# Optimization experiments

Measured on AMD Instinct MI355X. Metric: run time of the kernel, lower is better.

The kernel has to match this reference:

```python
import jax, jax.numpy as jnp
import numpy as np

N_CHANNELS = 256
N_NEIGHBOURS = 262144
DIM = 3


def setup_inputs() -> dict:
    key = jax.random.key(0)
    k1, k2, k3 = jax.random.split(key, 3)
    h = jax.random.normal(k1, (N_CHANNELS, N_NEIGHBOURS), dtype=jnp.float32)
    rel_poss = jax.random.normal(k2, (DIM, N_NEIGHBOURS), dtype=jnp.float32)
    W = jax.random.normal(k3, (N_CHANNELS, N_CHANNELS), dtype=jnp.float32)
    return {"h": h, "rel_poss": rel_poss, "W": W}


def reference(h, rel_poss, W):
    # dists: [N], unit directions u: [dim, N]
    dists = jnp.linalg.norm(rel_poss, axis=0)
    u = rel_poss / dists
    # radial basis e_rbf(x, n, c=2) = (2/2)**0.5 * sin(n*x)/x = sin(n*x)/x, n = 1..K
    n = jnp.arange(1, N_CHANNELS + 1, dtype=h.dtype)
    radial_emb = jnp.sin(n[:, None] * dists[None, :]) / dists[None, :]  # [K, N]
    # channel-mixed features
    hp = W @ h  # [K, N]
    # per-neighbour: radial * feature scalar times rank-2 outer product u u^T, summed over neighbours
    m = radial_emb * hp  # [K, N]
    A = jnp.einsum('ki,di,ei->kde', m, u, u)  # [K, dim, dim]
    return A
```

## Files before the change

kernel.cpp:

```cpp
#include <hip/hip_runtime.h>
#include <hip/hip_bf16.h>

#define NCH      256
#define NNB      262144
#define BN       64
#define NTILES   (NNB / BN)
#define NB       512
#define ITPB     (NTILES / NB)
#define NENT     (NCH * 6)
#define NTHREADS 512

typedef __bf16        bf16x8 __attribute__((ext_vector_type(8)));
typedef float         f32x4  __attribute__((ext_vector_type(4)));
typedef unsigned int  u32x4  __attribute__((ext_vector_type(4)));
typedef unsigned int  u32x2  __attribute__((ext_vector_type(2)));
typedef short         v4s    __attribute__((ext_vector_type(4)));

union FragU  { u32x4 u; bf16x8 b; };
union Frag2U { u32x2 u; v4s    s; };

__device__ __forceinline__ unsigned pk2(float lo, float hi) {
    union { __hip_bfloat162 h2; unsigned u; } cv;
    cv.h2 = __float22bfloat162_rn(make_float2(lo, hi));
    return cv.u;
}

__device__ __forceinline__ const float* uni_ptr(const float* p) {
    unsigned long long u = (unsigned long long)p;
    unsigned lo = __builtin_amdgcn_readfirstlane((unsigned)u);
    unsigned hi = __builtin_amdgcn_readfirstlane((unsigned)(u >> 32));
    return (const float*)(((unsigned long long)hi << 32) | lo);
}

#define LBAR() do {                                                  \
    asm volatile("s_waitcnt lgkmcnt(0)" ::: "memory");               \
    __builtin_amdgcn_sched_barrier(0);                               \
    __builtin_amdgcn_s_barrier();                                    \
    __builtin_amdgcn_sched_barrier(0);                               \
} while (0)

#define CBODY(CB, P)                                                               \
{                                                                                  \
    const int colb = (CB) * 16;                                                    \
    Frag2U gf;                                                                     \
    gf.u = *(const u32x2*)((const char*)gT[P] +                                    \
           (((unsigned)(il * 128 + (colb + q * 4) * 2)) ^                          \
            (((unsigned)(il & 7)) << 3)));                                         \
    f32x4 hp0 = {0.f, 0.f, 0.f, 0.f}, hp1 = {0.f, 0.f, 0.f, 0.f};                  \
    const unsigned rb = (unsigned)((colb + il) * 512);                             \
    const unsigned sw = ((unsigned)(il & 7)) << 4;                                 \
    _Pragma("unroll")                                                              \
    for (int jb = 0; jb < 8; ++jb) {                                               \
        FragU f0;                                                                  \
        f0.u = *(const u32x4*)((const char*)htile[P] +                             \
               ((rb + (unsigned)(jb * 64 + q * 16)) ^ sw));                        \
        hp0 = __builtin_amdgcn_mfma_f32_16x16x32_bf16(f0.b, wf[0][jb].b, hp0, 0, 0, 0); \
        hp1 = __builtin_amdgcn_mfma_f32_16x16x32_bf16(f0.b, wf[1][jb].b, hp1, 0, 0, 0); \
    }                                                                              \
    f32x4 d4 = *(const f32x4*)&dtab[P][0][colb + q * 4];                           \
    f32x4 i4 = *(const f32x4*)&dtab[P][1][colb + q * 4];                           \
    Frag2U a0, a1;                                                                 \
    {                                                                              \
        float m0 = __sinf(fk0 * d4[0]) * i4[0] * hp0[0];                           \
        float m1 = __sinf(fk0 * d4[1]) * i4[1] * hp0[1];                           \
        float m2 = __sinf(fk0 * d4[2]) * i4[2] * hp0[2];                           \
        float m3 = __sinf(fk0 * d4[3]) * i4[3] * hp0[3];                           \
        a0.u[0] = pk2(m0, m1); a0.u[1] = pk2(m2, m3);                              \
        float n0 = __sinf(fk1 * d4[0]) * i4[0] * hp1[0];                           \
        float n1 = __sinf(fk1 * d4[1]) * i4[1] * hp1[1];                           \
        float n2 = __sinf(fk1 * d4[2]) * i4[2] * hp1[2];                           \
        float n3 = __sinf(fk1 * d4[3]) * i4[3] * hp1[3];                           \
        a1.u[0] = pk2(n0, n1); a1.u[1] = pk2(n2, n3);                              \
    }                                                                              \
    acc0 = __builtin_amdgcn_mfma_f32_16x16x16bf16_1k(a0.s, gf.s, acc0, 0, 0, 0);   \
    acc1 = __builtin_amdgcn_mfma_f32_16x16x16bf16_1k(a1.s, gf.s, acc1, 0, 0, 0);   \
}

#define ITER(P, CUR, NXT, TILE_EXPR)                                               \
{                                                                                  \
    const int tile = (TILE_EXPR);                                                  \
    const int tn1  = tile + NB;                                                    \
    const int tn2  = tile + 2 * NB;                                                \
    const unsigned ii1 = (unsigned)(((tn1 < NTILES) ? tn1 : tile) * BN) + (unsigned)c; \
    {                                                    \
        const int lt = (tn2 < NTILES) ? tn2 : tile;                                \
        const unsigned ii = (unsigned)(lt * BN) + (unsigned)c;                     \
        NXT[0] = rp[ii];                                                           \
        NXT[1] = rp[(size_t)NNB + ii];                                             \
        NXT[2] = rp[2 * (size_t)NNB + ii];                                         \
    }                                                                              \
    float hA[16];                                                                  \
    if (tn1 < NTILES) {         \
        _Pragma("unroll")                                                          \
        for (int j = 0; j < 16; ++j) hA[j] = hwb[(size_t)j * NNB + ii1];           \
    }                                                                              \
    __builtin_amdgcn_sched_barrier(0);                                             \
    CBODY(0, P)                                                                    \
    CBODY(1, P)                                                                    \
    __builtin_amdgcn_sched_barrier(0);                                             \
    float hB[16];                                                                  \
    if (tn1 < NTILES) {                                                            \
                       \
        u32x4 w0, w1;                                                              \
        w0[0] = pk2(hA[0], hA[1]);   w0[1] = pk2(hA[2], hA[3]);                    \
        w0[2] = pk2(hA[4], hA[5]);   w0[3] = pk2(hA[6], hA[7]);                    \
        w1[0] = pk2(hA[8], hA[9]);   w1[1] = pk2(hA[10], hA[11]);                  \
        w1[2] = pk2(hA[12], hA[13]); w1[3] = pk2(hA[14], hA[15]);                  \
        const unsigned swc = ((unsigned)(c & 7)) << 4;                             \
        *(u32x4*)((char*)htile[(P) ^ 1] +                                          \
                  (((unsigned)(c * 512 + wave * 64)) ^ swc)) = w0;                 \
        *(u32x4*)((char*)htile[(P) ^ 1] +                                          \
                  (((unsigned)(c * 512 + wave * 64 + 16)) ^ swc)) = w1;            \
        _Pragma("unroll")                                                          \
        for (int j = 0; j < 16; ++j) hB[j] = hwb[(size_t)(16 + j) * NNB + ii1];    \
    }                                                                              \
    __builtin_amdgcn_sched_barrier(0);                                             \
    CBODY(2, P)                                                                    \
    CBODY(3, P)                                                                    \
    __builtin_amdgcn_sched_barrier(0);                                             \
    if (tn1 < NTILES) {      \
        u32x4 w2, w3;                                                              \
        w2[0] = pk2(hB[0], hB[1]);   w2[1] = pk2(hB[2], hB[3]);                    \
        w2[2] = pk2(hB[4], hB[5]);   w2[3] = pk2(hB[6], hB[7]);                    \
        w3[0] = pk2(hB[8], hB[9]);   w3[1] = pk2(hB[10], hB[11]);                  \
        w3[2] = pk2(hB[12], hB[13]); w3[3] = pk2(hB[14], hB[15]);                  \
        const unsigned swc = ((unsigned)(c & 7)) << 4;                             \
        *(u32x4*)((char*)htile[(P) ^ 1] +                                          \
                  (((unsigned)(c * 512 + wave * 64 + 32)) ^ swc)) = w2;            \
        *(u32x4*)((char*)htile[(P) ^ 1] +                                          \
                  (((unsigned)(c * 512 + wave * 64 + 48)) ^ swc)) = w3;            \
        float dd = sqrtf(CUR[0] * CUR[0] + CUR[1] * CUR[1] + CUR[2] * CUR[2]);     \
        float iv = 1.0f / dd;                                                      \
        if (t < 64) {                                                              \
            dtab[(P) ^ 1][0][c] = dd;                                              \
            dtab[(P) ^ 1][1][c] = iv;                                              \
            float i2 = iv * iv;                                                    \
            float gg[6] = { CUR[0] * CUR[0] * i2, CUR[0] * CUR[1] * i2,            \
                            CUR[0] * CUR[2] * i2, CUR[1] * CUR[1] * i2,            \
                            CUR[1] * CUR[2] * i2, CUR[2] * CUR[2] * i2 };          \
            _Pragma("unroll")                                                      \
            for (int de = 0; de < 6; ++de) {                                       \
                unsigned off = ((unsigned)(de * 128 + c * 2)) ^                    \
                               (((unsigned)de) << 3);                              \
                *(unsigned short*)((char*)gT[(P) ^ 1] + off) =                     \
                    (unsigned short)(pk2(gg[de], 0.f) & 0xffffu);                  \
            }                                                                      \
        }                                                                          \
    }                                                                              \
    LBAR();                                                                        \
}

__global__ __launch_bounds__(NTHREADS, 2) void create_As_k1(
        const float* __restrict__ h, const float* __restrict__ rp,
        const float* __restrict__ W, float* __restrict__ ws)
{
    __shared__ unsigned short htile[2][BN * NCH];
    __shared__ unsigned short gT[2][16 * BN];
    __shared__ __align__(16) float dtab[2][2][BN];

    const int t    = threadIdx.x;
    const int wave = t >> 6;
    const int il   = t & 15;
    const int q    = (t >> 4) & 3;
    const int c    = t & 63;
    const int k0   = wave * 32;
    const float fk0 = (float)(k0 + il + 1);
    const float fk1 = fk0 + 16.0f;

    #pragma unroll
    for (int z = 0; z < 4; ++z) ((unsigned*)gT)[t + z * NTHREADS] = 0u;

    FragU wf[2][8];
    #pragma unroll
    for (int kt = 0; kt < 2; ++kt) {
        const float* wr = W + (size_t)(k0 + kt * 16 + il) * NCH + q * 8;
        #pragma unroll
        for (int jb = 0; jb < 8; ++jb) {
            f32x4 a = *(const f32x4*)(wr + jb * 32);
            f32x4 b = *(const f32x4*)(wr + jb * 32 + 4);
            wf[kt][jb].u[0] = pk2(a[0], a[1]);
            wf[kt][jb].u[1] = pk2(a[2], a[3]);
            wf[kt][jb].u[2] = pk2(b[0], b[1]);
            wf[kt][jb].u[3] = pk2(b[2], b[3]);
        }
    }

    f32x4 acc0 = {0.f, 0.f, 0.f, 0.f};
    f32x4 acc1 = {0.f, 0.f, 0.f, 0.f};

    const float* hwb = uni_ptr(h + (size_t)(wave * 32) * NNB);

    float pA[3], pB[3];
    const int tile0 = blockIdx.x;

    __syncthreads();

    {
        const unsigned ii = (unsigned)(tile0 * BN) + (unsigned)c;
        pB[0] = rp[ii]; pB[1] = rp[(size_t)NNB + ii]; pB[2] = rp[2 * (size_t)NNB + ii];
        float hv[32];
        #pragma unroll
        for (int j = 0; j < 32; ++j) hv[j] = hwb[(size_t)j * NNB + ii];

        const unsigned swc = ((unsigned)(c & 7)) << 4;
        #pragma unroll
        for (int g2 = 0; g2 < 4; ++g2) {
            u32x4 w0;
            w0[0] = pk2(hv[g2 * 8 + 0], hv[g2 * 8 + 1]);
            w0[1] = pk2(hv[g2 * 8 + 2], hv[g2 * 8 + 3]);
            w0[2] = pk2(hv[g2 * 8 + 4], hv[g2 * 8 + 5]);
            w0[3] = pk2(hv[g2 * 8 + 6], hv[g2 * 8 + 7]);
            *(u32x4*)((char*)htile[0] +
                      (((unsigned)(c * 512 + wave * 64 + g2 * 16)) ^ swc)) = w0;
        }

        float dd = sqrtf(pB[0] * pB[0] + pB[1] * pB[1] + pB[2] * pB[2]);
        float iv = 1.0f / dd;
        if (t < 64) {
            dtab[0][0][c] = dd; dtab[0][1][c] = iv;
            float i2 = iv * iv;
            float gg[6] = { pB[0] * pB[0] * i2, pB[0] * pB[1] * i2, pB[0] * pB[2] * i2,
                            pB[1] * pB[1] * i2, pB[1] * pB[2] * i2, pB[2] * pB[2] * i2 };
            #pragma unroll
            for (int de = 0; de < 6; ++de) {
                unsigned off = ((unsigned)(de * 128 + c * 2)) ^ (((unsigned)de) << 3);
                *(unsigned short*)((char*)gT[0] + off) =
                    (unsigned short)(pk2(gg[de], 0.f) & 0xffffu);
            }
        }
        const unsigned i1 = (unsigned)((tile0 + NB) * BN) + (unsigned)c;
        pA[0] = rp[i1]; pA[1] = rp[(size_t)NNB + i1]; pA[2] = rp[2 * (size_t)NNB + i1];
    }
    LBAR();

    #pragma unroll 1
    for (int it2 = 0; it2 < ITPB; it2 += 2) {
        const int tb = tile0 + it2 * NB;
        ITER(0, pA, pB, tb)
        ITER(1, pB, pA, tb + NB)
    }

    if (il < 6) {
        float* dst = ws + (size_t)blockIdx.x * NENT;
        #pragma unroll
        for (int r = 0; r < 4; ++r) {
            dst[(k0 + q * 4 + r) * 6 + il]      = acc0[r];
            dst[(k0 + 16 + q * 4 + r) * 6 + il] = acc1[r];
        }
    }
}

__global__ void create_As_k2(const float* __restrict__ ws, float* __restrict__ out)
{
    __shared__ float red[8][64];
    const int eb = blockIdx.x;
    const int w  = threadIdx.x >> 6;
    const int l  = threadIdx.x & 63;
    float s = 0.f;
    #pragma unroll 4
    for (int b = w; b < NB; b += 8)
        s += ws[(size_t)b * NENT + (unsigned)(eb * 64 + l)];
    red[w][l] = s;
    __syncthreads();
    if (w == 0) {
        float v = red[0][l] + red[1][l] + red[2][l] + red[3][l]
                + red[4][l] + red[5][l] + red[6][l] + red[7][l];
        const int e  = eb * 64 + l;
        const int k  = e / 6;
        const int m6 = e - k * 6;
        const int d  = (m6 < 3) ? 0 : ((m6 < 5) ? 1 : 2);
        const int e2 = (m6 < 3) ? m6 : ((m6 < 5) ? (m6 - 2) : 2);
        out[k * 9 + d * 3 + e2] = v;
        if (d != e2) out[k * 9 + e2 * 3 + d] = v;
    }
}

extern "C" void kernel_launch(void* const* d_in, const int* in_sizes, int n_in,
                              void* d_out, int out_size, void* d_ws, size_t ws_size,
                              hipStream_t stream)
{
    const float* h  = (const float*)d_in[0];
    const float* rp = (const float*)d_in[1];
    const float* W  = (const float*)d_in[2];
    float* out = (float*)d_out;
    float* ws  = (float*)d_ws;

    hipLaunchKernelGGL(create_As_k1, dim3(NB), dim3(NTHREADS), 0, stream, h, rp, W, ws);
    hipLaunchKernelGGL(create_As_k2, dim3(NENT / 64), dim3(512), 0, stream, ws, out);
}
```

Baseline: 84.01 us.

## Double neighbour tile to 128 with one resident block per CU

Result: slower. 209.9 us (+149.8%).

```diff
diff --git a/kernel.cpp b/kernel.cpp
--- a/kernel.cpp
+++ b/kernel.cpp
@@ -3,10 +3,10 @@
 
 #define NCH      256
 #define NNB      262144
-#define BN       64
-#define NTILES   (NNB / BN)
-#define NB       512
-#define ITPB     (NTILES / NB)
+#define BN       128
+#define NDT      (NNB / BN)
+#define NB       256
+#define DTPB     (NDT / NB)
 #define NENT     (NCH * 6)
 #define NTHREADS 512
 
@@ -44,7 +44,7 @@
     const int colb = (CB) * 16;                                                    \
     Frag2U gf;                                                                     \
     gf.u = *(const u32x2*)((const char*)gT[P] +                                    \
-           (((unsigned)(il * 128 + (colb + q * 4) * 2)) ^                          \
+           (((unsigned)(il * 256 + (colb + q * 4) * 2)) ^                          \
             (((unsigned)(il & 7)) << 3)));                                         \
     f32x4 hp0 = {0.f, 0.f, 0.f, 0.f}, hp1 = {0.f, 0.f, 0.f, 0.f};                  \
     const unsigned rb = (unsigned)((colb + il) * 512);                             \
@@ -76,71 +76,66 @@
     acc1 = __builtin_amdgcn_mfma_f32_16x16x16bf16_1k(a1.s, gf.s, acc1, 0, 0, 0);   \
 }
 
-#define ITER(P, CUR, NXT, TILE_EXPR)                                               \
+#define ITER(P, CUR, NXT, DT_EXPR)                                                 \
 {                                                                                  \
-    const int tile = (TILE_EXPR);                                                  \
-    const int tn1  = tile + NB;                                                    \
-    const int tn2  = tile + 2 * NB;                                                \
-    const unsigned ii1 = (unsigned)(((tn1 < NTILES) ? tn1 : tile) * BN) + (unsigned)c; \
+    const int dt  = (DT_EXPR);                                                     \
+    const int dn1 = dt + NB;                                                       \
+    const int dn2 = dt + 2 * NB;                                                   \
+    const unsigned base1 = (unsigned)(((dn1 < NDT) ? dn1 : dt) * BN);              \
     {                                                    \
-        const int lt = (tn2 < NTILES) ? tn2 : tile;                                \
-        const unsigned ii = (unsigned)(lt * BN) + (unsigned)c;                     \
+        const int lt = (dn2 < NDT) ? dn2 : dt;                                     \
+        const unsigned ii = (unsigned)(lt * BN) + (unsigned)(t & 127);             \
         NXT[0] = rp[ii];                                                           \
         NXT[1] = rp[(size_t)NNB + ii];                                             \
         NXT[2] = rp[2 * (size_t)NNB + ii];                                         \
     }                                                                              \
-    float hA[16];                                                                  \
-    if (tn1 < NTILES) {         \
+    float hv0[32], hv1[32];                                                        \
+    if (dn1 < NDT) {                                                               \
         _Pragma("unroll")                                                          \
-        for (int j = 0; j < 16; ++j) hA[j] = hwb[(size_t)j * NNB + ii1];           \
+        for (int j = 0; j < 32; ++j) {                                             \
+            hv0[j] = hwb[(size_t)j * NNB + base1 + l];                             \
+            hv1[j] = hwb[(size_t)j * NNB + base1 + l + 64];                        \
+        }                                                                          \
     }                                                                              \
     __builtin_amdgcn_sched_barrier(0);                                             \
-    CBODY(0, P)                                                                    \
-    CBODY(1, P)                                                                    \
+    CBODY(0, P) CBODY(1, P) CBODY(2, P) CBODY(3, P)                                \
+    CBODY(4, P) CBODY(5, P) CBODY(6, P) CBODY(7, P)                                \
     __builtin_amdgcn_sched_barrier(0);                                             \
-    float hB[16];                                                                  \
-    if (tn1 < NTILES) {                                                            \
-                       \
-        u32x4 w0, w1;                                                              \
-        w0[0] = pk2(hA[0], hA[1]);   w0[1] = pk2(hA[2], hA[3]);                    \
-        w0[2] = pk2(hA[4], hA[5]);   w0[3] = pk2(hA[6], hA[7]);                    \
-        w1[0] = pk2(hA[8], hA[9]);   w1[1] = pk2(hA[10], hA[11]);                  \
-        w1[2] = pk2(hA[12], hA[13]); w1[3] = pk2(hA[14], hA[15]);                  \
-        const unsigned swc = ((unsigned)(c & 7)) << 4;                             \
-        *(u32x4*)((char*)htile[(P) ^ 1] +                                          \
-                  (((unsigned)(c * 512 + wave * 64)) ^ swc)) = w0;                 \
-        *(u32x4*)((char*)htile[(P) ^ 1] +                                          \
-                  (((unsigned)(c * 512 + wave * 64 + 16)) ^ swc)) = w1;            \
+    if (dn1 < NDT) {                                                               \
+        const unsigned swp = ((unsigned)(l & 7)) << 4;                             \
         _Pragma("unroll")                                                          \
-        for (int j = 0; j < 16; ++j) hB[j] = hwb[(size_t)(16 + j) * NNB + ii1];    \
-    }                                                                              \
-    __builtin_amdgcn_sched_barrier(0);                                             \
-    CBODY(2, P)                                                                    \
-    CBODY(3, P)                                                                    \
-    __builtin_amdgcn_sched_barrier(0);                                             \
-    if (tn1 < NTILES) {      \
-        u32x4 w2, w3;                                                              \
-        w2[0] = pk2(hB[0], hB[1]);   w2[1] = pk2(hB[2], hB[3]);                    \
-        w2[2] = pk2(hB[4], hB[5]);   w2[3] = pk2(hB[6], hB[7]);                    \
-        w3[0] = pk2(hB[8], hB[9]);   w3[1] = pk2(hB[10], hB[11]);                  \
-        w3[2] = pk2(hB[12], hB[13]); w3[3] = pk2(hB[14], hB[15]);                  \
-        const unsigned swc = ((unsigned)(c & 7)) << 4;                             \
-        *(u32x4*)((char*)htile[(P) ^ 1] +                                          \
-                  (((unsigned)(c * 512 + wave * 64 + 32)) ^ swc)) = w2;            \
-        *(u32x4*)((char*)htile[(P) ^ 1] +                                          \
-                  (((unsigned)(c * 512 + wave * 64 + 48)) ^ swc)) = w3;            \
-        float dd = sqrtf(CUR[0] * CUR[0] + CUR[1] * CUR[1] + CUR[2] * CUR[2]);     \
-        float iv = 1.0f / dd;                                                      \
-        if (t < 64) {                                                              \
-            dtab[(P) ^ 1][0][c] = dd;                                              \
-            dtab[(P) ^ 1][1][c] = iv;                                              \
+        for (int g2 = 0; g2 < 4; ++g2) {                                           \
+            u32x4 w0;                                                              \
+            w0[0] = pk2(hv0[g2 * 8 + 0], hv0[g2 * 8 + 1]);                         \
+            w0[1] = pk2(hv0[g2 * 8 + 2], hv0[g2 * 8 + 3]);                         \
+            w0[2] = pk2(hv0[g2 * 8 + 4], hv0[g2 * 8 + 5]);                         \
+            w0[3] = pk2(hv0[g2 * 8 + 6], hv0[g2 * 8 + 7]);                         \
+            *(u32x4*)((char*)htile[(P) ^ 1] +                                      \
+                      (((unsigned)(l * 512 + wave * 64 + g2 * 16)) ^ swp)) = w0;   \
+        }                                                                          \
+        _Pragma("unroll")                                                          \
+        for (int g2 = 0; g2 < 4; ++g2) {                                           \
+            u32x4 w1;                                                              \
+            w1[0] = pk2(hv1[g2 * 8 + 0], hv1[g2 * 8 + 1]);                         \
+            w1[1] = pk2(hv1[g2 * 8 + 2], hv1[g2 * 8 + 3]);                         \
+            w1[2] = pk2(hv1[g2 * 8 + 4], hv1[g2 * 8 + 5]);                         \
+            w1[3] = pk2(hv1[g2 * 8 + 6], hv1[g2 * 8 + 7]);                         \
+            *(u32x4*)((char*)htile[(P) ^ 1] +                                      \
+                      (((unsigned)((l + 64) * 512 + wave * 64 + g2 * 16)) ^ swp)) = w1; \
+        }                                                                          \
+        if (t < 128) {                        \
+            const int cc = t;                                                      \
+            float dd = sqrtf(CUR[0] * CUR[0] + CUR[1] * CUR[1] + CUR[2] * CUR[2]); \
+            float iv = 1.0f / dd;                                                  \
+            dtab[(P) ^ 1][0][cc] = dd;                                             \
+            dtab[(P) ^ 1][1][cc] = iv;                                             \
             float i2 = iv * iv;                                                    \
             float gg[6] = { CUR[0] * CUR[0] * i2, CUR[0] * CUR[1] * i2,            \
                             CUR[0] * CUR[2] * i2, CUR[1] * CUR[1] * i2,            \
                             CUR[1] * CUR[2] * i2, CUR[2] * CUR[2] * i2 };          \
             _Pragma("unroll")                                                      \
             for (int de = 0; de < 6; ++de) {                                       \
-                unsigned off = ((unsigned)(de * 128 + c * 2)) ^                    \
+                unsigned off = ((unsigned)(de * 256 + cc * 2)) ^                   \
                                (((unsigned)de) << 3);                              \
                 *(unsigned short*)((char*)gT[(P) ^ 1] + off) =                     \
                     (unsigned short)(pk2(gg[de], 0.f) & 0xffffu);                  \
@@ -150,7 +145,7 @@
     LBAR();                                                                        \
 }
 
-__global__ __launch_bounds__(NTHREADS, 2) void create_As_k1(
+__global__ __launch_bounds__(NTHREADS, 1) void create_As_k1(
         const float* __restrict__ h, const float* __restrict__ rp,
         const float* __restrict__ W, float* __restrict__ ws)
 {
@@ -160,15 +155,15 @@
 
     const int t    = threadIdx.x;
     const int wave = t >> 6;
+    const int l    = t & 63;
     const int il   = t & 15;
     const int q    = (t >> 4) & 3;
-    const int c    = t & 63;
     const int k0   = wave * 32;
     const float fk0 = (float)(k0 + il + 1);
     const float fk1 = fk0 + 16.0f;
 
     #pragma unroll
-    for (int z = 0; z < 4; ++z) ((unsigned*)gT)[t + z * NTHREADS] = 0u;
+    for (int z = 0; z < 8; ++z) ((unsigned*)gT)[t + z * NTHREADS] = 0u;
 
     FragU wf[2][8];
     #pragma unroll
@@ -191,53 +186,66 @@
     const float* hwb = uni_ptr(h + (size_t)(wave * 32) * NNB);
 
     float pA[3], pB[3];
-    const int tile0 = blockIdx.x;
+    const int d0 = blockIdx.x;
 
     __syncthreads();
 
     {
-        const unsigned ii = (unsigned)(tile0 * BN) + (unsigned)c;
+        const unsigned ii = (unsigned)(d0 * BN) + (unsigned)(t & 127);
         pB[0] = rp[ii]; pB[1] = rp[(size_t)NNB + ii]; pB[2] = rp[2 * (size_t)NNB + ii];
-        float hv[32];
-        #pragma unroll
-        for (int j = 0; j < 32; ++j) hv[j] = hwb[(size_t)j * NNB + ii];
-
-        const unsigned swc = ((unsigned)(c & 7)) << 4;
+        const unsigned base = (unsigned)(d0 * BN);
+        float hv0[32], hv1[32];
+        #pragma unroll
+        for (int j = 0; j < 32; ++j) {
+            hv0[j] = hwb[(size_t)j * NNB + base + l];
+            hv1[j] = hwb[(size_t)j * NNB + base + l + 64];
+        }
+        const unsigned swp = ((unsigned)(l & 7)) << 4;
         #pragma unroll
         for (int g2 = 0; g2 < 4; ++g2) {
             u32x4 w0;
-            w0[0] = pk2(hv[g2 * 8 + 0], hv[g2 * 8 + 1]);
-            w0[1] = pk2(hv[g2 * 8 + 2], hv[g2 * 8 + 3]);
-            w0[2] = pk2(hv[g2 * 8 + 4], hv[g2 * 8 + 5]);
-            w0[3] = pk2(hv[g2 * 8 + 6], hv[g2 * 8 + 7]);
+            w0[0] = pk2(hv0[g2 * 8 + 0], hv0[g2 * 8 + 1]);
+            w0[1] = pk2(hv0[g2 * 8 + 2], hv0[g2 * 8 + 3]);
+            w0[2] = pk2(hv0[g2 * 8 + 4], hv0[g2 * 8 + 5]);
+            w0[3] = pk2(hv0[g2 * 8 + 6], hv0[g2 * 8 + 7]);
             *(u32x4*)((char*)htile[0] +
-                      (((unsigned)(c * 512 + wave * 64 + g2 * 16)) ^ swc)) = w0;
-        }
-
-        float dd = sqrtf(pB[0] * pB[0] + pB[1] * pB[1] + pB[2] * pB[2]);
-        float iv = 1.0f / dd;
-        if (t < 64) {
-            dtab[0][0][c] = dd; dtab[0][1][c] = iv;
+                      (((unsigned)(l * 512 + wave * 64 + g2 * 16)) ^ swp)) = w0;
+        }
+        #pragma unroll
+        for (int g2 = 0; g2 < 4; ++g2) {
+            u32x4 w1;
+            w1[0] = pk2(hv1[g2 * 8 + 0], hv1[g2 * 8 + 1]);
+            w1[1] = pk2(hv1[g2 * 8 + 2], hv1[g2 * 8 + 3]);
+            w1[2] = pk2(hv1[g2 * 8 + 4], hv1[g2 * 8 + 5]);
+            w1[3] = pk2(hv1[g2 * 8 + 6], hv1[g2 * 8 + 7]);
+            *(u32x4*)((char*)htile[0] +
+                      (((unsigned)((l + 64) * 512 + wave * 64 + g2 * 16)) ^ swp)) = w1;
+        }
+        if (t < 128) {
+            const int cc = t;
+            float dd = sqrtf(pB[0] * pB[0] + pB[1] * pB[1] + pB[2] * pB[2]);
+            float iv = 1.0f / dd;
+            dtab[0][0][cc] = dd; dtab[0][1][cc] = iv;
             float i2 = iv * iv;
             float gg[6] = { pB[0] * pB[0] * i2, pB[0] * pB[1] * i2, pB[0] * pB[2] * i2,
                             pB[1] * pB[1] * i2, pB[1] * pB[2] * i2, pB[2] * pB[2] * i2 };
             #pragma unroll
             for (int de = 0; de < 6; ++de) {
-                unsigned off = ((unsigned)(de * 128 + c * 2)) ^ (((unsigned)de) << 3);
+                unsigned off = ((unsigned)(de * 256 + cc * 2)) ^ (((unsigned)de) << 3);
                 *(unsigned short*)((char*)gT[0] + off) =
                     (unsigned short)(pk2(gg[de], 0.f) & 0xffffu);
             }
         }
-        const unsigned i1 = (unsigned)((tile0 + NB) * BN) + (unsigned)c;
+        const unsigned i1 = (unsigned)((d0 + NB) * BN) + (unsigned)(t & 127);
         pA[0] = rp[i1]; pA[1] = rp[(size_t)NNB + i1]; pA[2] = rp[2 * (size_t)NNB + i1];
     }
     LBAR();
 
     #pragma unroll 1
-    for (int it2 = 0; it2 < ITPB; it2 += 2) {
-        const int tb = tile0 + it2 * NB;
-        ITER(0, pA, pB, tb)
-        ITER(1, pB, pA, tb + NB)
+    for (int it2 = 0; it2 < DTPB; it2 += 2) {
+        const int db = d0 + it2 * NB;
+        ITER(0, pA, pB, db)
+        ITER(1, pB, pA, db + NB)
     }
 
     if (il < 6) {
```

## Prefetch next h tile in four 8-channel chunks interleaved with compute

Applied to the files above, without the earlier changes.

New measurement: 83.42 us. No clear change (-0.7%).

```diff
diff --git a/kernel.cpp b/kernel.cpp
--- a/kernel.cpp
+++ b/kernel.cpp
@@ -39,26 +39,25 @@
     __builtin_amdgcn_sched_barrier(0);                               \
 } while (0)
 
-#define CBODY(CB, P)                                                               \
+#define CBODY(CB)                                                                  \
 {                                                                                  \
     const int colb = (CB) * 16;                                                    \
     Frag2U gf;                                                                     \
-    gf.u = *(const u32x2*)((const char*)gT[P] +                                    \
+    gf.u = *(const u32x2*)(gTP +                                                   \
            (((unsigned)(il * 128 + (colb + q * 4) * 2)) ^                          \
             (((unsigned)(il & 7)) << 3)));                                         \
     f32x4 hp0 = {0.f, 0.f, 0.f, 0.f}, hp1 = {0.f, 0.f, 0.f, 0.f};                  \
     const unsigned rb = (unsigned)((colb + il) * 512);                             \
-    const unsigned sw = ((unsigned)(il & 7)) << 4;                                 \
     _Pragma("unroll")                                                              \
     for (int jb = 0; jb < 8; ++jb) {                                               \
         FragU f0;                                                                  \
-        f0.u = *(const u32x4*)((const char*)htile[P] +                             \
+        f0.u = *(const u32x4*)((const char*)htP +                                  \
                ((rb + (unsigned)(jb * 64 + q * 16)) ^ sw));                        \
         hp0 = __builtin_amdgcn_mfma_f32_16x16x32_bf16(f0.b, wf[0][jb].b, hp0, 0, 0, 0); \
         hp1 = __builtin_amdgcn_mfma_f32_16x16x32_bf16(f0.b, wf[1][jb].b, hp1, 0, 0, 0); \
     }                                                                              \
-    f32x4 d4 = *(const f32x4*)&dtab[P][0][colb + q * 4];                           \
-    f32x4 i4 = *(const f32x4*)&dtab[P][1][colb + q * 4];                           \
+    f32x4 d4 = *(const f32x4*)(dtP + colb + q * 4);                                \
+    f32x4 i4 = *(const f32x4*)(dtP + 64 + colb + q * 4);                           \
     Frag2U a0, a1;                                                                 \
     {                                                                              \
         float m0 = __sinf(fk0 * d4[0]) * i4[0] * hp0[0];                           \
@@ -76,79 +75,21 @@
     acc1 = __builtin_amdgcn_mfma_f32_16x16x16bf16_1k(a1.s, gf.s, acc1, 0, 0, 0);   \
 }
 
-#define ITER(P, CUR, NXT, TILE_EXPR)                                               \
-{                                                                                  \
-    const int tile = (TILE_EXPR);                                                  \
-    const int tn1  = tile + NB;                                                    \
-    const int tn2  = tile + 2 * NB;                                                \
-    const unsigned ii1 = (unsigned)(((tn1 < NTILES) ? tn1 : tile) * BN) + (unsigned)c; \
-    {                                                    \
-        const int lt = (tn2 < NTILES) ? tn2 : tile;                                \
-        const unsigned ii = (unsigned)(lt * BN) + (unsigned)c;                     \
-        NXT[0] = rp[ii];                                                           \
-        NXT[1] = rp[(size_t)NNB + ii];                                             \
-        NXT[2] = rp[2 * (size_t)NNB + ii];                                         \
-    }                                                                              \
-    float hA[16];                                                                  \
-    if (tn1 < NTILES) {         \
+#define CHUNK8_ISSUE(Q)                                                            \
+    if (hasNext) {                                                                 \
         _Pragma("unroll")                                                          \
-        for (int j = 0; j < 16; ++j) hA[j] = hwb[(size_t)j * NNB + ii1];           \
-    }                                                                              \
-    __builtin_amdgcn_sched_barrier(0);                                             \
-    CBODY(0, P)                                                                    \
-    CBODY(1, P)                                                                    \
-    __builtin_amdgcn_sched_barrier(0);                                             \
-    float hB[16];                                                                  \
-    if (tn1 < NTILES) {                                                            \
-                       \
-        u32x4 w0, w1;                                                              \
-        w0[0] = pk2(hA[0], hA[1]);   w0[1] = pk2(hA[2], hA[3]);                    \
-        w0[2] = pk2(hA[4], hA[5]);   w0[3] = pk2(hA[6], hA[7]);                    \
-        w1[0] = pk2(hA[8], hA[9]);   w1[1] = pk2(hA[10], hA[11]);                  \
-        w1[2] = pk2(hA[12], hA[13]); w1[3] = pk2(hA[14], hA[15]);                  \
-        const unsigned swc = ((unsigned)(c & 7)) << 4;                             \
-        *(u32x4*)((char*)htile[(P) ^ 1] +                                          \
-                  (((unsigned)(c * 512 + wave * 64)) ^ swc)) = w0;                 \
-        *(u32x4*)((char*)htile[(P) ^ 1] +                                          \
-                  (((unsigned)(c * 512 + wave * 64 + 16)) ^ swc)) = w1;            \
-        _Pragma("unroll")                                                          \
-        for (int j = 0; j < 16; ++j) hB[j] = hwb[(size_t)(16 + j) * NNB + ii1];    \
-    }                                                                              \
-    __builtin_amdgcn_sched_barrier(0);                                             \
-    CBODY(2, P)                                                                    \
-    CBODY(3, P)                                                                    \
-    __builtin_amdgcn_sched_barrier(0);                                             \
-    if (tn1 < NTILES) {      \
-        u32x4 w2, w3;                                                              \
-        w2[0] = pk2(hB[0], hB[1]);   w2[1] = pk2(hB[2], hB[3]);                    \
-        w2[2] = pk2(hB[4], hB[5]);   w2[3] = pk2(hB[6], hB[7]);                    \
-        w3[0] = pk2(hB[8], hB[9]);   w3[1] = pk2(hB[10], hB[11]);                  \
-        w3[2] = pk2(hB[12], hB[13]); w3[3] = pk2(hB[14], hB[15]);                  \
-        const unsigned swc = ((unsigned)(c & 7)) << 4;                             \
-        *(u32x4*)((char*)htile[(P) ^ 1] +                                          \
-                  (((unsigned)(c * 512 + wave * 64 + 32)) ^ swc)) = w2;            \
-        *(u32x4*)((char*)htile[(P) ^ 1] +                                          \
-                  (((unsigned)(c * 512 + wave * 64 + 48)) ^ swc)) = w3;            \
-        float dd = sqrtf(CUR[0] * CUR[0] + CUR[1] * CUR[1] + CUR[2] * CUR[2]);     \
-        float iv = 1.0f / dd;                                                      \
-        if (t < 64) {                                                              \
-            dtab[(P) ^ 1][0][c] = dd;                                              \
-            dtab[(P) ^ 1][1][c] = iv;                                              \
-            float i2 = iv * iv;                                                    \
-            float gg[6] = { CUR[0] * CUR[0] * i2, CUR[0] * CUR[1] * i2,            \
-                            CUR[0] * CUR[2] * i2, CUR[1] * CUR[1] * i2,            \
-                            CUR[1] * CUR[2] * i2, CUR[2] * CUR[2] * i2 };          \
-            _Pragma("unroll")                                                      \
-            for (int de = 0; de < 6; ++de) {                                       \
-                unsigned off = ((unsigned)(de * 128 + c * 2)) ^                    \
-                               (((unsigned)de) << 3);                              \
-                *(unsigned short*)((char*)gT[(P) ^ 1] + off) =                     \
-                    (unsigned short)(pk2(gg[de], 0.f) & 0xffffu);                  \
-            }                                                                      \
-        }                                                                          \
-    }                                                                              \
-    LBAR();                                                                        \
-}
+        for (int j = 0; j < 8; ++j)                                                \
+            hc[j] = hwb[(size_t)((Q) * 8 + j) * NNB + baseN + c];                  \
+    }
+
+#define CHUNK8_PACK(Q)                                                             \
+    if (hasNext) {                                                                 \
+        u32x4 w0;                                                                  \
+        w0[0] = pk2(hc[0], hc[1]); w0[1] = pk2(hc[2], hc[3]);                      \
+        w0[2] = pk2(hc[4], hc[5]); w0[3] = pk2(hc[6], hc[7]);                      \
+        *(u32x4*)((char*)htN +                                                     \
+            (((unsigned)(c * 512 + wave * 64 + (Q) * 16)) ^ swc)) = w0;            \
+    }
 
 __global__ __launch_bounds__(NTHREADS, 2) void create_As_k1(
         const float* __restrict__ h, const float* __restrict__ rp,
@@ -164,11 +105,13 @@
     const int q    = (t >> 4) & 3;
     const int c    = t & 63;
     const int k0   = wave * 32;
+    const unsigned sw  = ((unsigned)(il & 7)) << 4;
+    const unsigned swc = ((unsigned)(c & 7)) << 4;
     const float fk0 = (float)(k0 + il + 1);
     const float fk1 = fk0 + 16.0f;
 
     #pragma unroll
-    for (int z = 0; z < 4; ++z) ((unsigned*)gT)[t + z * NTHREADS] = 0u;
+    for (int z = 0; z < 2; ++z) ((unsigned*)gT)[t + z * NTHREADS] = 0u;
 
     FragU wf[2][8];
     #pragma unroll
@@ -190,37 +133,33 @@
 
     const float* hwb = uni_ptr(h + (size_t)(wave * 32) * NNB);
 
-    float pA[3], pB[3];
-    const int tile0 = blockIdx.x;
+    const int d0 = blockIdx.x;
 
     __syncthreads();
 
     {
-        const unsigned ii = (unsigned)(tile0 * BN) + (unsigned)c;
-        pB[0] = rp[ii]; pB[1] = rp[(size_t)NNB + ii]; pB[2] = rp[2 * (size_t)NNB + ii];
-        float hv[32];
+        const unsigned base = (unsigned)(d0 * BN);
         #pragma unroll
-        for (int j = 0; j < 32; ++j) hv[j] = hwb[(size_t)j * NNB + ii];
-
-        const unsigned swc = ((unsigned)(c & 7)) << 4;
-        #pragma unroll
-        for (int g2 = 0; g2 < 4; ++g2) {
+        for (int qq = 0; qq < 4; ++qq) {
+            float hv[8];
+            #pragma unroll
+            for (int j = 0; j < 8; ++j)
+                hv[j] = hwb[(size_t)(qq * 8 + j) * NNB + base + c];
             u32x4 w0;
-            w0[0] = pk2(hv[g2 * 8 + 0], hv[g2 * 8 + 1]);
-            w0[1] = pk2(hv[g2 * 8 + 2], hv[g2 * 8 + 3]);
-            w0[2] = pk2(hv[g2 * 8 + 4], hv[g2 * 8 + 5]);
-            w0[3] = pk2(hv[g2 * 8 + 6], hv[g2 * 8 + 7]);
+            w0[0] = pk2(hv[0], hv[1]); w0[1] = pk2(hv[2], hv[3]);
+            w0[2] = pk2(hv[4], hv[5]); w0[3] = pk2(hv[6], hv[7]);
             *(u32x4*)((char*)htile[0] +
-                      (((unsigned)(c * 512 + wave * 64 + g2 * 16)) ^ swc)) = w0;
-        }
-
-        float dd = sqrtf(pB[0] * pB[0] + pB[1] * pB[1] + pB[2] * pB[2]);
-        float iv = 1.0f / dd;
+                (((unsigned)(c * 512 + wave * 64 + qq * 16)) ^ swc)) = w0;
+        }
         if (t < 64) {
+            const unsigned ii = base + (unsigned)c;
+            float gx = rp[ii], gy = rp[(size_t)NNB + ii], gz = rp[2 * (size_t)NNB + ii];
+            float dd = sqrtf(gx * gx + gy * gy + gz * gz);
+            float iv = 1.0f / dd;
             dtab[0][0][c] = dd; dtab[0][1][c] = iv;
             float i2 = iv * iv;
-            float gg[6] = { pB[0] * pB[0] * i2, pB[0] * pB[1] * i2, pB[0] * pB[2] * i2,
-                            pB[1] * pB[1] * i2, pB[1] * pB[2] * i2, pB[2] * pB[2] * i2 };
+            float gg[6] = { gx * gx * i2, gx * gy * i2, gx * gz * i2,
+                            gy * gy * i2, gy * gz * i2, gz * gz * i2 };
             #pragma unroll
             for (int de = 0; de < 6; ++de) {
                 unsigned off = ((unsigned)(de * 128 + c * 2)) ^ (((unsigned)de) << 3);
@@ -228,16 +167,58 @@
                     (unsigned short)(pk2(gg[de], 0.f) & 0xffffu);
             }
         }
-        const unsigned i1 = (unsigned)((tile0 + NB) * BN) + (unsigned)c;
-        pA[0] = rp[i1]; pA[1] = rp[(size_t)NNB + i1]; pA[2] = rp[2 * (size_t)NNB + i1];
     }
     LBAR();
 
     #pragma unroll 1
-    for (int it2 = 0; it2 < ITPB; it2 += 2) {
-        const int tb = tile0 + it2 * NB;
-        ITER(0, pA, pB, tb)
-        ITER(1, pB, pA, tb + NB)
+    for (int it = 0; it < ITPB; ++it) {
+        const int P = it & 1;
+        const unsigned short* htP = htile[P];
+        unsigned short*       htN = htile[P ^ 1];
+        const char*  gTP = (const char*)gT[P];
+        const float* dtP = &dtab[P][0][0];
+        const bool hasNext = (it + 1 < ITPB);
+        const unsigned baseN = (unsigned)((d0 + (it + 1) * NB) * BN);
+
+        float gx = 0.f, gy = 0.f, gz = 0.f;
+        if (hasNext && t < 64) {
+            const unsigned ii = baseN + (unsigned)c;
+            gx = rp[ii]; gy = rp[(size_t)NNB + ii]; gz = rp[2 * (size_t)NNB + ii];
+        }
+
+        float hc[8];
+        CHUNK8_ISSUE(0)
+        __builtin_amdgcn_sched_barrier(0);
+        CBODY(0)
+        __builtin_amdgcn_sched_barrier(0);
+        CHUNK8_PACK(0) CHUNK8_ISSUE(1)
+        __builtin_amdgcn_sched_barrier(0);
+        CBODY(1)
+        __builtin_amdgcn_sched_barrier(0);
+        CHUNK8_PACK(1) CHUNK8_ISSUE(2)
+        __builtin_amdgcn_sched_barrier(0);
+        CBODY(2)
+        __builtin_amdgcn_sched_barrier(0);
+        CHUNK8_PACK(2) CHUNK8_ISSUE(3)
+        __builtin_amdgcn_sched_barrier(0);
+        CBODY(3)
+        __builtin_amdgcn_sched_barrier(0);
+        CHUNK8_PACK(3)
+        if (hasNext && t < 64) {
+            float dd = sqrtf(gx * gx + gy * gy + gz * gz);
+            float iv = 1.0f / dd;
+            dtab[P ^ 1][0][c] = dd; dtab[P ^ 1][1][c] = iv;
+            float i2 = iv * iv;
+            float gg[6] = { gx * gx * i2, gx * gy * i2, gx * gz * i2,
+                            gy * gy * i2, gy * gz * i2, gz * gz * i2 };
+            #pragma unroll
+            for (int de = 0; de < 6; ++de) {
+                unsigned off = ((unsigned)(de * 128 + c * 2)) ^ (((unsigned)de) << 3);
+                *(unsigned short*)((char*)gT[P ^ 1] + off) =
+                    (unsigned short)(pk2(gg[de], 0.f) & 0xffffu);
+            }
+        }
+        LBAR();
     }
 
     if (il < 6) {
```
